# Optimization experiments

Hardware: AMD Instinct MI355X
Metric: run time of the kernel (lower is better)

## Reference

```python
import jax, jax.numpy as jnp
import numpy as np

B, P, D_IN = 128, 4096, 4   # frames, points/frame, xyz+time
NG = 16                      # number of trajectory groups
H1, H2, H3 = 64, 128, 512    # PointNet shared-MLP widths


def _init_mlp(key, dims):
    ks = jax.random.split(key, len(dims) - 1)
    params = []
    for k, (di, do) in zip(ks, zip(dims[:-1], dims[1:])):
        W = jax.random.normal(k, (di, do), dtype=jnp.float32) * (1.0 / np.sqrt(di))
        b = jnp.zeros((do,), dtype=jnp.float32)
        params.append((W, b))
    return params


def setup_inputs() -> dict:
    key = jax.random.key(0)
    k_pc, k_t, k_idx, k_g, k_l = jax.random.split(key, 5)
    pc = jax.random.normal(k_pc, (B, 3, P), dtype=jnp.float32)
    traj_time_batch = jax.random.uniform(k_t, (B, 1), dtype=jnp.float32)
    traj_inbatch_index = jnp.sort(jax.random.randint(k_idx, (B,), 0, NG)).astype(jnp.int32)
    (Wg1, bg1), (Wg2, bg2), (Wg3, bg3) = _init_mlp(k_g, [D_IN, H1, H2, H3])
    (Wl1, bl1), (Wl2, bl2), (Wl3, bl3) = _init_mlp(k_l, [D_IN, H1, H2, H3])
    return dict(pc=pc, traj_time_batch=traj_time_batch, traj_inbatch_index=traj_inbatch_index,
                Wg1=Wg1, bg1=bg1, Wg2=Wg2, bg2=bg2, Wg3=Wg3, bg3=bg3,
                Wl1=Wl1, bl1=bl1, Wl2=Wl2, bl2=bl2, Wl3=Wl3, bl3=bl3)


def _mlp(x, layers):
    # pointwise shared MLP: x [..., P, d_in] -> [..., P, d_out]
    for W, b in layers:
        x = jax.nn.relu(x @ W + b)
    return x


def reference(pc, traj_time_batch, traj_inbatch_index,
              Wg1, bg1, Wg2, bg2, Wg3, bg3,
              Wl1, bl1, Wl2, bl2, Wl3, bl3):
    b, _, p = pc.shape
    # append time channel: [B,3,P] + [B,1,P] -> [B,4,P]
    t = jnp.broadcast_to(traj_time_batch[..., None], (b, 1, p))
    feat = jnp.concatenate([pc, t], axis=1)
    x = jnp.swapaxes(feat, 1, 2)  # [B,P,4] points-last layout for pointwise MLP

    # global branch: shared MLP on every point, then max over all points of each trajectory group
    hg = _mlp(x, [(Wg1, bg1), (Wg2, bg2), (Wg3, bg3)])           # [B,P,H3]
    seg = jnp.repeat(traj_inbatch_index, p)                       # [B*P]
    gmax = jax.ops.segment_max(hg.reshape(b * p, -1), seg, num_segments=NG)  # [NG,H3]
    global_feat = gmax[traj_inbatch_index]                        # [B,H3] broadcast back per frame

    # local branch: per-frame PointNet encode (shared MLP + max over points)
    hl = _mlp(x, [(Wl1, bl1), (Wl2, bl2), (Wl3, bl3)])            # [B,P,H3]
    local_feat = hl.max(axis=1)                                   # [B,H3]

    z = jnp.concatenate([global_feat, local_feat], axis=1)        # [B,2*H3]
    input_features_vis = pc                                       # original pc (last dim == 4096, no slice)
    return (z, input_features_vis)
```

## Files before the change

### kernel.cpp

```cpp
#include <hip/hip_runtime.h>
#include <hip/hip_bf16.h>

#define NB   128
#define NP   4096
#define NGRP 16
#define C3   512

typedef __bf16 bf16x8 __attribute__((ext_vector_type(8)));
typedef __bf16 bf16x4 __attribute__((ext_vector_type(4)));
typedef float  f32x4  __attribute__((ext_vector_type(4)));

#define WS_W1T_G 0
#define WS_W1T_L 4096
#define WS_W2T_G 8192
#define WS_W2T_L 24576
#define WS_W3T_G 40960
#define WS_W3T_L 172032
#define WS_GMAX  303104

#define H1_S 72
#define H2_S 136

__global__ void prep_kernel(const float* __restrict__ Wg1, const float* __restrict__ Wg2,
                            const float* __restrict__ Wg3, const float* __restrict__ Wl1,
                            const float* __restrict__ Wl2, const float* __restrict__ Wl3,
                            float* __restrict__ out, char* __restrict__ ws) {
    int gid = blockIdx.x * blockDim.x + threadIdx.x;
    out[gid] = 0.0f;
    float* gmax = (float*)(ws + WS_GMAX);
    if (gid < NGRP * C3) gmax[gid] = 0.0f;
    __bf16* w1tg = (__bf16*)(ws + WS_W1T_G);
    __bf16* w1tl = (__bf16*)(ws + WS_W1T_L);
    __bf16* w2tg = (__bf16*)(ws + WS_W2T_G);
    __bf16* w2tl = (__bf16*)(ws + WS_W2T_L);
    __bf16* w3tg = (__bf16*)(ws + WS_W3T_G);
    __bf16* w3tl = (__bf16*)(ws + WS_W3T_L);
    if (gid < 64 * 32) {
        int ch = gid >> 5, k = gid & 31;
        w1tg[gid] = (k < 4) ? (__bf16)Wg1[k * 64 + ch] : (__bf16)0.0f;
        w1tl[gid] = (k < 4) ? (__bf16)Wl1[k * 64 + ch] : (__bf16)0.0f;
    }
    if (gid < 128 * 64) {
        int ch = gid >> 6, k = gid & 63;
        w2tg[gid] = (__bf16)Wg2[k * 128 + ch];
        w2tl[gid] = (__bf16)Wl2[k * 128 + ch];
    }
    if (gid < 512 * 128) {
        int ch = gid >> 7, k = gid & 127;
        w3tg[gid] = (__bf16)Wg3[k * 512 + ch];
        w3tl[gid] = (__bf16)Wl3[k * 512 + ch];
    }
}

__global__ __launch_bounds__(512, 2) void main_kernel(
    const float* __restrict__ pc, const float* __restrict__ tt, const int* __restrict__ idx,
    const float* __restrict__ bg1, const float* __restrict__ bg2, const float* __restrict__ bg3,
    const float* __restrict__ bl1, const float* __restrict__ bl2, const float* __restrict__ bl3,
    float* __restrict__ out, char* __restrict__ ws) {
    __shared__ __align__(16) char smem[78848];
    __bf16* h1 = (__bf16*)smem;
    __bf16* h2 = (__bf16*)(smem + 9216);

    const int tid    = threadIdx.x;
    const int lane   = tid & 63;
    const int wave   = tid >> 6;
    const int quad   = lane >> 4;
    const int l15    = lane & 15;
    const int branch = blockIdx.y;
    const int chunk  = blockIdx.x;
    const int frame  = chunk >> 2;
    const int p0     = (chunk & 3) * 1024;

    const __bf16* w1t = (const __bf16*)(ws + (branch ? WS_W1T_L : WS_W1T_G));
    const __bf16* w2t = (const __bf16*)(ws + (branch ? WS_W2T_L : WS_W2T_G));
    const __bf16* w3t = (const __bf16*)(ws + (branch ? WS_W3T_L : WS_W3T_G));
    const float* b1 = branch ? bl1 : bg1;
    const float* b2 = branch ? bl2 : bg2;
    const float* b3 = branch ? bl3 : bg3;

    const int ni1  = wave >> 1;
    const int mi1  = (wave & 1) * 2;
    const int chb2 = wave * 16;
    const int ch3  = wave * 64;

    bf16x8 a1[2];
    #pragma unroll
    for (int mm = 0; mm < 2; ++mm)
        a1[mm] = *(const bf16x8*)(w1t + ((mi1 + mm) * 16 + l15) * 32 + quad * 8);
    bf16x8 a2[2];
    #pragma unroll
    for (int ks = 0; ks < 2; ++ks)
        a2[ks] = *(const bf16x8*)(w2t + (chb2 + l15) * 64 + ks * 32 + quad * 8);
    bf16x8 aw[4][4];
    #pragma unroll
    for (int mi = 0; mi < 4; ++mi)
        #pragma unroll
        for (int ks = 0; ks < 4; ++ks)
            aw[mi][ks] = *(const bf16x8*)(w3t + (ch3 + mi * 16 + l15) * 128 + ks * 32 + quad * 8);

    float b1r[2][4], b2r[4];
    #pragma unroll
    for (int mm = 0; mm < 2; ++mm)
        #pragma unroll
        for (int r = 0; r < 4; ++r) b1r[mm][r] = b1[(mi1 + mm) * 16 + quad * 4 + r];
    #pragma unroll
    for (int r = 0; r < 4; ++r) b2r[r] = b2[chb2 + quad * 4 + r];

    const float tval = tt[frame];
    const f32x4 zf = {0.0f, 0.0f, 0.0f, 0.0f};
    f32x4 runmax[4];
    #pragma unroll
    for (int mi = 0; mi < 4; ++mi) runmax[mi] = (f32x4){-1e30f, -1e30f, -1e30f, -1e30f};

    const float* pcx = pc + (size_t)frame * 3 * NP;

    for (int m = 0; m < 4; ++m) {
        float xf[4][3];
        const int pb = p0 + m * 256 + ni1 * 16 + l15;
        #pragma unroll
        for (int s = 0; s < 4; ++s) {
            xf[s][0] = pcx[pb + s * 64];
            xf[s][1] = pcx[NP + pb + s * 64];
            xf[s][2] = pcx[2 * NP + pb + s * 64];
        }

        #pragma unroll
        for (int s = 0; s < 4; ++s) {
            bf16x8 xb;
            #pragma unroll
            for (int j = 0; j < 8; ++j) xb[j] = (__bf16)0.0f;
            if (quad == 0) {
                xb[0] = (__bf16)xf[s][0]; xb[1] = (__bf16)xf[s][1];
                xb[2] = (__bf16)xf[s][2]; xb[3] = (__bf16)tval;
            }
            #pragma unroll
            for (int mm = 0; mm < 2; ++mm) {
                f32x4 c = __builtin_amdgcn_mfma_f32_16x16x32_bf16(a1[mm], xb, zf, 0, 0, 0);
                bf16x4 pk;
                #pragma unroll
                for (int r = 0; r < 4; ++r) pk[r] = (__bf16)fmaxf(c[r] + b1r[mm][r], 0.0f);
                *(bf16x4*)(h1 + (ni1 * 16 + l15) * H1_S + (mi1 + mm) * 16 + quad * 4) = pk;
            }
            __syncthreads();
            #pragma unroll
            for (int ni = 0; ni < 4; ++ni) {
                bf16x8 q0 = *(const bf16x8*)(h1 + (ni * 16 + l15) * H1_S + quad * 8);
                bf16x8 q1 = *(const bf16x8*)(h1 + (ni * 16 + l15) * H1_S + 32 + quad * 8);
                f32x4 c = __builtin_amdgcn_mfma_f32_16x16x32_bf16(a2[0], q0, zf, 0, 0, 0);
                c = __builtin_amdgcn_mfma_f32_16x16x32_bf16(a2[1], q1, c, 0, 0, 0);
                bf16x4 pk;
                #pragma unroll
                for (int r = 0; r < 4; ++r) pk[r] = (__bf16)fmaxf(c[r] + b2r[r], 0.0f);
                *(bf16x4*)(h2 + (s * 64 + ni * 16 + l15) * H2_S + chb2 + quad * 4) = pk;
            }
            __syncthreads();
        }

        bf16x8 bh[4], bhn[4];
        #pragma unroll
        for (int ks = 0; ks < 4; ++ks)
            bh[ks] = *(const bf16x8*)(h2 + l15 * H2_S + ks * 32 + quad * 8);
        #pragma unroll 4
        for (int ni = 0; ni < 16; ++ni) {
            const int nin = (ni + 1) & 15;
            #pragma unroll
            for (int ks = 0; ks < 4; ++ks)
                bhn[ks] = *(const bf16x8*)(h2 + (nin * 16 + l15) * H2_S + ks * 32 + quad * 8);
            f32x4 acc[4];
            #pragma unroll
            for (int ks = 0; ks < 4; ++ks)
                #pragma unroll
                for (int mi = 0; mi < 4; ++mi)
                    acc[mi] = __builtin_amdgcn_mfma_f32_16x16x32_bf16(
                        aw[mi][ks], bh[ks], ks ? acc[mi] : zf, 0, 0, 0);
            #pragma unroll
            for (int mi = 0; mi < 4; ++mi)
                #pragma unroll
                for (int r = 0; r < 4; ++r)
                    runmax[mi][r] = fmaxf(runmax[mi][r], acc[mi][r]);
            #pragma unroll
            for (int ks = 0; ks < 4; ++ks) bh[ks] = bhn[ks];
        }
    }

    const int g = idx[frame];
    float* gmax = (float*)(ws + WS_GMAX);
    unsigned* dst = (branch == 0) ? (unsigned*)(gmax + g * C3)
                                  : (unsigned*)(out + frame * (2 * C3) + C3);
    #pragma unroll
    for (int mi = 0; mi < 4; ++mi) {
        f32x4 v = runmax[mi];
        #pragma unroll
        for (int d = 1; d < 16; d <<= 1) {
            #pragma unroll
            for (int r = 0; r < 4; ++r) v[r] = fmaxf(v[r], __shfl_xor(v[r], d));
        }
        if (l15 == 0) {
            #pragma unroll
            for (int r = 0; r < 4; ++r) {
                int ch = ch3 + mi * 16 + quad * 4 + r;
                float fv = fmaxf(v[r] + b3[ch], 0.0f);
                atomicMax(dst + ch, __float_as_uint(fv));
            }
        }
    }
}

__global__ void gather_kernel(const int* __restrict__ idx, const char* __restrict__ ws,
                              float* __restrict__ out) {
    int i = blockIdx.x * blockDim.x + threadIdx.x;
    int b = i >> 9, ch = i & 511;
    const float* gmax = (const float*)(ws + WS_GMAX);
    out[b * (2 * C3) + ch] = gmax[idx[b] * C3 + ch];
}

extern "C" void kernel_launch(void* const* d_in, const int* in_sizes, int n_in,
                              void* d_out, int out_size, void* d_ws, size_t ws_size,
                              hipStream_t stream) {
    const float* pc  = (const float*)d_in[0];
    const float* tt  = (const float*)d_in[1];
    const int*   idx = (const int*)d_in[2];
    const float* Wg1 = (const float*)d_in[3];  const float* bg1 = (const float*)d_in[4];
    const float* Wg2 = (const float*)d_in[5];  const float* bg2 = (const float*)d_in[6];
    const float* Wg3 = (const float*)d_in[7];  const float* bg3 = (const float*)d_in[8];
    const float* Wl1 = (const float*)d_in[9];  const float* bl1 = (const float*)d_in[10];
    const float* Wl2 = (const float*)d_in[11]; const float* bl2 = (const float*)d_in[12];
    const float* Wl3 = (const float*)d_in[13]; const float* bl3 = (const float*)d_in[14];
    float* out = (float*)d_out;
    char*  ws  = (char*)d_ws;

    hipMemcpyAsync(out + NB * 2 * C3, pc, (size_t)NB * 3 * NP * sizeof(float),
                   hipMemcpyDeviceToDevice, stream);
    prep_kernel<<<512, 256, 0, stream>>>(Wg1, Wg2, Wg3, Wl1, Wl2, Wl3, out, ws);
    main_kernel<<<dim3(512, 2), 512, 0, stream>>>(pc, tt, idx, bg1, bg2, bg3,
                                                  bl1, bl2, bl3, out, ws);
    gather_kernel<<<256, 256, 0, stream>>>(idx, ws, out);
}
```

Baseline: 233.0 us.

## Restructure PointNet kernel: per-frame blocks, fragment-layout weights, pipelined layer overlap

Prep now writes weights pre-swizzled into MFMA fragment order through an LDS transpose tile, and it also performs the pc copy itself instead of a separate memcpy. The main kernel uses one block per frame per branch (256 blocks instead of 1024), keeps W2 in shared memory, and double-buffers layer-2 activations. Layers 1 and 2 for the next 128-point chunk are interleaved with the layer-3 MFMA loop. The local branch writes its result directly instead of using an atomic. This cuts barriers and weight reloads, but the smaller grid may underfill the GPU's CUs and the larger LDS use lowers occupancy.

```diff
diff --git a/kernel.cpp b/kernel.cpp
--- a/kernel.cpp
+++ b/kernel.cpp
@@ -10,45 +10,75 @@
 typedef __bf16 bf16x4 __attribute__((ext_vector_type(4)));
 typedef float  f32x4  __attribute__((ext_vector_type(4)));
 
-#define WS_W1T_G 0
-#define WS_W1T_L 4096
-#define WS_W2T_G 8192
-#define WS_W2T_L 24576
-#define WS_W3T_G 40960
-#define WS_W3T_L 172032
+#define WS_W1F_G 0
+#define WS_W1F_L 4096
+#define WS_W2F_G 8192
+#define WS_W2F_L 24576
+#define WS_W3F_G 40960
+#define WS_W3F_L 172032
 #define WS_GMAX  303104
 
-#define H1_S 72
-#define H2_S 136
-
-__global__ void prep_kernel(const float* __restrict__ Wg1, const float* __restrict__ Wg2,
-                            const float* __restrict__ Wg3, const float* __restrict__ Wl1,
-                            const float* __restrict__ Wl2, const float* __restrict__ Wl3,
-                            float* __restrict__ out, char* __restrict__ ws) {
-    int gid = blockIdx.x * blockDim.x + threadIdx.x;
-    out[gid] = 0.0f;
-    float* gmax = (float*)(ws + WS_GMAX);
-    if (gid < NGRP * C3) gmax[gid] = 0.0f;
-    __bf16* w1tg = (__bf16*)(ws + WS_W1T_G);
-    __bf16* w1tl = (__bf16*)(ws + WS_W1T_L);
-    __bf16* w2tg = (__bf16*)(ws + WS_W2T_G);
-    __bf16* w2tl = (__bf16*)(ws + WS_W2T_L);
-    __bf16* w3tg = (__bf16*)(ws + WS_W3T_G);
-    __bf16* w3tl = (__bf16*)(ws + WS_W3T_L);
-    if (gid < 64 * 32) {
-        int ch = gid >> 5, k = gid & 31;
-        w1tg[gid] = (k < 4) ? (__bf16)Wg1[k * 64 + ch] : (__bf16)0.0f;
-        w1tl[gid] = (k < 4) ? (__bf16)Wl1[k * 64 + ch] : (__bf16)0.0f;
-    }
-    if (gid < 128 * 64) {
-        int ch = gid >> 6, k = gid & 63;
-        w2tg[gid] = (__bf16)Wg2[k * 128 + ch];
-        w2tl[gid] = (__bf16)Wl2[k * 128 + ch];
-    }
-    if (gid < 512 * 128) {
-        int ch = gid >> 7, k = gid & 127;
-        w3tg[gid] = (__bf16)Wg3[k * 512 + ch];
-        w3tl[gid] = (__bf16)Wl3[k * 512 + ch];
+__global__ __launch_bounds__(256) void prep_kernel(
+    const float* __restrict__ Wg1, const float* __restrict__ Wg2, const float* __restrict__ Wg3,
+    const float* __restrict__ Wl1, const float* __restrict__ Wl2, const float* __restrict__ Wl3,
+    const float* __restrict__ pc, float* __restrict__ out, char* __restrict__ ws) {
+    const int t = blockIdx.x, tid = threadIdx.x;
+    if (t >= 37) {
+        const f32x4* src = (const f32x4*)pc;
+        f32x4* dst = (f32x4*)(out + NB * 2 * C3);
+        int base = (t - 37) * 1024 + tid;
+        #pragma unroll
+        for (int j = 0; j < 4; ++j) dst[base + j * 256] = src[base + j * 256];
+        return;
+    }
+    if (t == 36) {
+        float* gmax = (float*)(ws + WS_GMAX);
+        #pragma unroll
+        for (int k = 0; k < 32; ++k) gmax[k * 256 + tid] = 0.0f;
+        int c = tid >> 6, lane = tid & 63;
+        int ch = c * 16 + (lane & 15);
+        int kb = (lane >> 4) * 8;
+        bf16x8 pg, pl;
+        #pragma unroll
+        for (int j = 0; j < 8; ++j) {
+            int k = kb + j;
+            pg[j] = (k < 4) ? (__bf16)Wg1[k * 64 + ch] : (__bf16)0.0f;
+            pl[j] = (k < 4) ? (__bf16)Wl1[k * 64 + ch] : (__bf16)0.0f;
+        }
+        *(bf16x8*)((__bf16*)(ws + WS_W1F_G) + c * 512 + lane * 8) = pg;
+        *(bf16x8*)((__bf16*)(ws + WS_W1F_L) + c * 512 + lane * 8) = pl;
+        return;
+    }
+    __shared__ float tile[64][65];
+    const float* src; __bf16* dst; int cBase, mMul, srcStride;
+    if (t < 32) {
+        int branch = t >> 4, rem = t & 15;
+        int tk = rem >> 3, tc = rem & 7;
+        src = (branch ? Wl3 : Wg3) + (size_t)(tk * 64) * 512 + tc * 64;
+        dst = (__bf16*)(ws + (branch ? WS_W3F_L : WS_W3F_G));
+        cBase = tc * 16 + tk * 2; mMul = 4; srcStride = 512;
+    } else {
+        int u = t - 32; int branch = u >> 1, tc = u & 1;
+        src = (branch ? Wl2 : Wg2) + tc * 64;
+        dst = (__bf16*)(ws + (branch ? WS_W2F_L : WS_W2F_G));
+        cBase = tc * 8; mMul = 2; srcStride = 128;
+    }
+    {
+        int r0 = tid >> 6, cl = tid & 63;
+        #pragma unroll
+        for (int p = 0; p < 16; ++p)
+            tile[p * 4 + r0][cl] = src[(size_t)(p * 4 + r0) * srcStride + cl];
+    }
+    __syncthreads();
+    int lane = tid & 63, l15 = lane & 15, q = lane >> 4;
+    #pragma unroll
+    for (int cc = 0; cc < 2; ++cc) {
+        int pair = (tid >> 6) * 2 + cc;
+        int mi = pair >> 1, ks = pair & 1;
+        bf16x8 pk;
+        #pragma unroll
+        for (int j = 0; j < 8; ++j) pk[j] = (__bf16)tile[ks * 32 + q * 8 + j][mi * 16 + l15];
+        *(bf16x8*)(dst + (cBase + mi * mMul + ks) * 512 + lane * 8) = pk;
     }
 }
 
@@ -57,54 +87,41 @@
     const float* __restrict__ bg1, const float* __restrict__ bg2, const float* __restrict__ bg3,
     const float* __restrict__ bl1, const float* __restrict__ bl2, const float* __restrict__ bl3,
     float* __restrict__ out, char* __restrict__ ws) {
-    __shared__ __align__(16) char smem[78848];
-    __bf16* h1 = (__bf16*)smem;
-    __bf16* h2 = (__bf16*)(smem + 9216);
-
-    const int tid    = threadIdx.x;
-    const int lane   = tid & 63;
-    const int wave   = tid >> 6;
-    const int quad   = lane >> 4;
-    const int l15    = lane & 15;
-    const int branch = blockIdx.y;
-    const int chunk  = blockIdx.x;
-    const int frame  = chunk >> 2;
-    const int p0     = (chunk & 3) * 1024;
-
-    const __bf16* w1t = (const __bf16*)(ws + (branch ? WS_W1T_L : WS_W1T_G));
-    const __bf16* w2t = (const __bf16*)(ws + (branch ? WS_W2T_L : WS_W2T_G));
-    const __bf16* w3t = (const __bf16*)(ws + (branch ? WS_W3T_L : WS_W3T_G));
+    __shared__ __align__(16) char smem[102912];
+    __bf16* h2f = (__bf16*)smem;
+    __bf16* w2f = (__bf16*)(smem + 65536);
+    __bf16* h1s = (__bf16*)(smem + 81920);
+    float*  b2s = (float*)(smem + 102400);
+
+    const int tid = threadIdx.x, lane = tid & 63, wave = tid >> 6;
+    const int quad = lane >> 4, l15 = lane & 15;
+    const int branch = blockIdx.y, frame = blockIdx.x;
+
+    const __bf16* w1g = (const __bf16*)(ws + (branch ? WS_W1F_L : WS_W1F_G));
+    const __bf16* w2g = (const __bf16*)(ws + (branch ? WS_W2F_L : WS_W2F_G));
+    const __bf16* w3g = (const __bf16*)(ws + (branch ? WS_W3F_L : WS_W3F_G));
     const float* b1 = branch ? bl1 : bg1;
     const float* b2 = branch ? bl2 : bg2;
     const float* b3 = branch ? bl3 : bg3;
 
-    const int ni1  = wave >> 1;
-    const int mi1  = (wave & 1) * 2;
-    const int chb2 = wave * 16;
-    const int ch3  = wave * 64;
-
-    bf16x8 a1[2];
-    #pragma unroll
-    for (int mm = 0; mm < 2; ++mm)
-        a1[mm] = *(const bf16x8*)(w1t + ((mi1 + mm) * 16 + l15) * 32 + quad * 8);
-    bf16x8 a2[2];
-    #pragma unroll
-    for (int ks = 0; ks < 2; ++ks)
-        a2[ks] = *(const bf16x8*)(w2t + (chb2 + l15) * 64 + ks * 32 + quad * 8);
+    for (int i = tid; i < 1024; i += 512) ((f32x4*)w2f)[i] = ((const f32x4*)w2g)[i];
+    if (tid < 128) b2s[tid] = b2[tid];
+
+    bf16x8 a1[4];
+    #pragma unroll
+    for (int mi = 0; mi < 4; ++mi) a1[mi] = *(const bf16x8*)(w1g + mi * 512 + lane * 8);
     bf16x8 aw[4][4];
     #pragma unroll
     for (int mi = 0; mi < 4; ++mi)
         #pragma unroll
         for (int ks = 0; ks < 4; ++ks)
-            aw[mi][ks] = *(const bf16x8*)(w3t + (ch3 + mi * 16 + l15) * 128 + ks * 32 + quad * 8);
-
-    float b1r[2][4], b2r[4];
-    #pragma unroll
-    for (int mm = 0; mm < 2; ++mm)
-        #pragma unroll
-        for (int r = 0; r < 4; ++r) b1r[mm][r] = b1[(mi1 + mm) * 16 + quad * 4 + r];
-    #pragma unroll
-    for (int r = 0; r < 4; ++r) b2r[r] = b2[chb2 + quad * 4 + r];
+            aw[mi][ks] = *(const bf16x8*)(w3g + (wave * 16 + mi * 4 + ks) * 512 + lane * 8);
+
+    float b1r[4][4];
+    #pragma unroll
+    for (int mi = 0; mi < 4; ++mi)
+        #pragma unroll
+        for (int r = 0; r < 4; ++r) b1r[mi][r] = b1[mi * 16 + quad * 4 + r];
 
     const float tval = tt[frame];
     const f32x4 zf = {0.0f, 0.0f, 0.0f, 0.0f};
@@ -113,80 +130,117 @@
     for (int mi = 0; mi < 4; ++mi) runmax[mi] = (f32x4){-1e30f, -1e30f, -1e30f, -1e30f};
 
     const float* pcx = pc + (size_t)frame * 3 * NP;
-
-    for (int m = 0; m < 4; ++m) {
-        float xf[4][3];
-        const int pb = p0 + m * 256 + ni1 * 16 + l15;
-        #pragma unroll
-        for (int s = 0; s < 4; ++s) {
-            xf[s][0] = pcx[pb + s * 64];
-            xf[s][1] = pcx[NP + pb + s * 64];
-            xf[s][2] = pcx[2 * NP + pb + s * 64];
-        }
-
-        #pragma unroll
-        for (int s = 0; s < 4; ++s) {
-            bf16x8 xb;
-            #pragma unroll
-            for (int j = 0; j < 8; ++j) xb[j] = (__bf16)0.0f;
-            if (quad == 0) {
-                xb[0] = (__bf16)xf[s][0]; xb[1] = (__bf16)xf[s][1];
-                xb[2] = (__bf16)xf[s][2]; xb[3] = (__bf16)tval;
-            }
-            #pragma unroll
-            for (int mm = 0; mm < 2; ++mm) {
-                f32x4 c = __builtin_amdgcn_mfma_f32_16x16x32_bf16(a1[mm], xb, zf, 0, 0, 0);
-                bf16x4 pk;
-                #pragma unroll
-                for (int r = 0; r < 4; ++r) pk[r] = (__bf16)fmaxf(c[r] + b1r[mm][r], 0.0f);
-                *(bf16x4*)(h1 + (ni1 * 16 + l15) * H1_S + (mi1 + mm) * 16 + quad * 4) = pk;
-            }
-            __syncthreads();
-            #pragma unroll
-            for (int ni = 0; ni < 4; ++ni) {
-                bf16x8 q0 = *(const bf16x8*)(h1 + (ni * 16 + l15) * H1_S + quad * 8);
-                bf16x8 q1 = *(const bf16x8*)(h1 + (ni * 16 + l15) * H1_S + 32 + quad * 8);
-                f32x4 c = __builtin_amdgcn_mfma_f32_16x16x32_bf16(a2[0], q0, zf, 0, 0, 0);
-                c = __builtin_amdgcn_mfma_f32_16x16x32_bf16(a2[1], q1, c, 0, 0, 0);
-                bf16x4 pk;
-                #pragma unroll
-                for (int r = 0; r < 4; ++r) pk[r] = (__bf16)fmaxf(c[r] + b2r[r], 0.0f);
-                *(bf16x4*)(h2 + (s * 64 + ni * 16 + l15) * H2_S + chb2 + quad * 4) = pk;
-            }
-            __syncthreads();
-        }
-
-        bf16x8 bh[4], bhn[4];
-        #pragma unroll
-        for (int ks = 0; ks < 4; ++ks)
-            bh[ks] = *(const bf16x8*)(h2 + l15 * H2_S + ks * 32 + quad * 8);
-        #pragma unroll 4
-        for (int ni = 0; ni < 16; ++ni) {
-            const int nin = (ni + 1) & 15;
-            #pragma unroll
-            for (int ks = 0; ks < 4; ++ks)
-                bhn[ks] = *(const bf16x8*)(h2 + (nin * 16 + l15) * H2_S + ks * 32 + quad * 8);
+    __bf16* hs = h1s + wave * 1280;
+    const int pw = wave * 16 + l15;
+
+    float xx = pcx[pw], xy = pcx[NP + pw], xz = pcx[2 * NP + pw];
+
+    __syncthreads();
+
+    {
+        bf16x8 xb;
+        #pragma unroll
+        for (int j = 0; j < 8; ++j) xb[j] = (__bf16)0.0f;
+        if (quad == 0) { xb[0] = (__bf16)xx; xb[1] = (__bf16)xy; xb[2] = (__bf16)xz; xb[3] = (__bf16)tval; }
+        #pragma unroll
+        for (int mi = 0; mi < 4; ++mi) {
+            f32x4 c = __builtin_amdgcn_mfma_f32_16x16x32_bf16(a1[mi], xb, zf, 0, 0, 0);
+            bf16x4 pk;
+            #pragma unroll
+            for (int r = 0; r < 4; ++r) pk[r] = (__bf16)fmaxf(c[r] + b1r[mi][r], 0.0f);
+            *(bf16x4*)(hs + l15 * 80 + mi * 16 + quad * 4) = pk;
+        }
+        bf16x8 hbf0 = *(const bf16x8*)(hs + l15 * 80 + quad * 8);
+        bf16x8 hbf1 = *(const bf16x8*)(hs + l15 * 80 + 32 + quad * 8);
+        #pragma unroll
+        for (int mi = 0; mi < 8; ++mi) {
+            bf16x8 a20 = *(const bf16x8*)(w2f + (mi * 2) * 512 + lane * 8);
+            bf16x8 a21 = *(const bf16x8*)(w2f + (mi * 2 + 1) * 512 + lane * 8);
+            f32x4 c = __builtin_amdgcn_mfma_f32_16x16x32_bf16(a20, hbf0, zf, 0, 0, 0);
+            c = __builtin_amdgcn_mfma_f32_16x16x32_bf16(a21, hbf1, c, 0, 0, 0);
+            f32x4 bb = *(const f32x4*)(b2s + mi * 16 + quad * 4);
+            bf16x4 pk;
+            #pragma unroll
+            for (int r = 0; r < 4; ++r) pk[r] = (__bf16)fmaxf(c[r] + bb[r], 0.0f);
+            const int c0 = mi * 16 + quad * 4;
+            *(bf16x4*)(h2f + ((wave * 4 + (c0 >> 5)) * 4 + ((c0 >> 3) & 3)) * 128 + l15 * 8 + (c0 & 7)) = pk;
+        }
+    }
+
+    for (int m = 0; m < 32; ++m) {
+        __syncthreads();
+        const __bf16* hb = h2f + (m & 1) * 16384;
+        __bf16* hbn = h2f + ((m + 1) & 1) * 16384;
+        const bool more = (m < 31);
+        float nx = 0.f, ny = 0.f, nz = 0.f;
+        if (more) {
+            const int p = (m + 1) * 128 + pw;
+            nx = pcx[p]; ny = pcx[NP + p]; nz = pcx[2 * NP + p];
+        }
+        bf16x8 hbf0, hbf1;
+        bf16x8 bh0[4], bh1[4];
+        #pragma unroll
+        for (int ks = 0; ks < 4; ++ks) bh0[ks] = *(const bf16x8*)(hb + ks * 512 + lane * 8);
+        #pragma unroll
+        for (int ni = 0; ni < 8; ++ni) {
+            bf16x8* cur = (ni & 1) ? bh1 : bh0;
+            bf16x8* nxt = (ni & 1) ? bh0 : bh1;
+            if (ni < 7) {
+                #pragma unroll
+                for (int ks = 0; ks < 4; ++ks)
+                    nxt[ks] = *(const bf16x8*)(hb + ((ni + 1) * 4 + ks) * 512 + lane * 8);
+            }
             f32x4 acc[4];
             #pragma unroll
             for (int ks = 0; ks < 4; ++ks)
                 #pragma unroll
                 for (int mi = 0; mi < 4; ++mi)
                     acc[mi] = __builtin_amdgcn_mfma_f32_16x16x32_bf16(
-                        aw[mi][ks], bh[ks], ks ? acc[mi] : zf, 0, 0, 0);
+                        aw[mi][ks], cur[ks], ks ? acc[mi] : zf, 0, 0, 0);
             #pragma unroll
             for (int mi = 0; mi < 4; ++mi)
                 #pragma unroll
                 for (int r = 0; r < 4; ++r)
                     runmax[mi][r] = fmaxf(runmax[mi][r], acc[mi][r]);
-            #pragma unroll
-            for (int ks = 0; ks < 4; ++ks) bh[ks] = bhn[ks];
+
+            if (more && ni == 2) {
+                bf16x8 xb;
+                #pragma unroll
+                for (int j = 0; j < 8; ++j) xb[j] = (__bf16)0.0f;
+                if (quad == 0) { xb[0] = (__bf16)nx; xb[1] = (__bf16)ny; xb[2] = (__bf16)nz; xb[3] = (__bf16)tval; }
+                #pragma unroll
+                for (int mi = 0; mi < 4; ++mi) {
+                    f32x4 c = __builtin_amdgcn_mfma_f32_16x16x32_bf16(a1[mi], xb, zf, 0, 0, 0);
+                    bf16x4 pk;
+                    #pragma unroll
+                    for (int r = 0; r < 4; ++r) pk[r] = (__bf16)fmaxf(c[r] + b1r[mi][r], 0.0f);
+                    *(bf16x4*)(hs + l15 * 80 + mi * 16 + quad * 4) = pk;
+                }
+            }
+            if (more && ni == 4) {
+                hbf0 = *(const bf16x8*)(hs + l15 * 80 + quad * 8);
+                hbf1 = *(const bf16x8*)(hs + l15 * 80 + 32 + quad * 8);
+            }
+            if (more && ni == 6) {
+                #pragma unroll
+                for (int mi = 0; mi < 8; ++mi) {
+                    bf16x8 a20 = *(const bf16x8*)(w2f + (mi * 2) * 512 + lane * 8);
+                    bf16x8 a21 = *(const bf16x8*)(w2f + (mi * 2 + 1) * 512 + lane * 8);
+                    f32x4 c = __builtin_amdgcn_mfma_f32_16x16x32_bf16(a20, hbf0, zf, 0, 0, 0);
+                    c = __builtin_amdgcn_mfma_f32_16x16x32_bf16(a21, hbf1, c, 0, 0, 0);
+                    f32x4 bb = *(const f32x4*)(b2s + mi * 16 + quad * 4);
+                    bf16x4 pk;
+                    #pragma unroll
+                    for (int r = 0; r < 4; ++r) pk[r] = (__bf16)fmaxf(c[r] + bb[r], 0.0f);
+                    const int c0 = mi * 16 + quad * 4;
+                    *(bf16x4*)(hbn + ((wave * 4 + (c0 >> 5)) * 4 + ((c0 >> 3) & 3)) * 128 + l15 * 8 + (c0 & 7)) = pk;
+                }
+            }
         }
     }
 
     const int g = idx[frame];
     float* gmax = (float*)(ws + WS_GMAX);
-    unsigned* dst = (branch == 0) ? (unsigned*)(gmax + g * C3)
-                                  : (unsigned*)(out + frame * (2 * C3) + C3);
     #pragma unroll
     for (int mi = 0; mi < 4; ++mi) {
         f32x4 v = runmax[mi];
@@ -198,9 +252,12 @@
         if (l15 == 0) {
             #pragma unroll
             for (int r = 0; r < 4; ++r) {
-                int ch = ch3 + mi * 16 + quad * 4 + r;
-                float fv = fmaxf(v[r] + b3[ch], 0.0f);
-                atomicMax(dst + ch, __float_as_uint(fv));
+                const int ch = wave * 64 + mi * 16 + quad * 4 + r;
+                const float fv = fmaxf(v[r] + b3[ch], 0.0f);
+                if (branch == 0)
+                    atomicMax((unsigned*)(gmax + g * C3 + ch), __float_as_uint(fv));
+                else
+                    out[(size_t)frame * (2 * C3) + C3 + ch] = fv;
             }
         }
     }
@@ -229,10 +286,8 @@
     float* out = (float*)d_out;
     char*  ws  = (char*)d_ws;
 
-    hipMemcpyAsync(out + NB * 2 * C3, pc, (size_t)NB * 3 * NP * sizeof(float),
-                   hipMemcpyDeviceToDevice, stream);
-    prep_kernel<<<512, 256, 0, stream>>>(Wg1, Wg2, Wg3, Wl1, Wl2, Wl3, out, ws);
-    main_kernel<<<dim3(512, 2), 512, 0, stream>>>(pc, tt, idx, bg1, bg2, bg3,
+    prep_kernel<<<421, 256, 0, stream>>>(Wg1, Wg2, Wg3, Wl1, Wl2, Wl3, pc, out, ws);
+    main_kernel<<<dim3(128, 2), 512, 0, stream>>>(pc, tt, idx, bg1, bg2, bg3,
                                                   bl1, bl2, bl3, out, ws);
     gather_kernel<<<256, 256, 0, stream>>>(idx, ws, out);
 }
```

Measured after the change: 202.2 us. 13.2% less time.
